# Kernel tuning notes

Hardware: AMD Instinct MI355X
Metric: run time of the kernel (lower is better)

The kernel has to match this reference:

```python
import jax, jax.numpy as jnp
import numpy as np

H, HKV, HD = 16, 4, 128
EPS = 1.1920928955078125e-07  # float32 eps, torch F.rms_norm default


def _rms_norm(t):
    return t * jax.lax.rsqrt(jnp.mean(t * t, axis=-1, keepdims=True) + EPS)


def _rope(t, cos, sin):
    # t: [B, T, h, HD]; cos/sin: [T, HD//2] -> broadcast [1, T, 1, HD//2]
    te, to = t[..., 0::2], t[..., 1::2]
    c = cos[None, :, None, :]
    s = sin[None, :, None, :]
    re = te * c - to * s
    ro = te * s + to * c
    return jnp.stack((re, ro), axis=-1).reshape(t.shape)


def setup_inputs() -> dict:
    key = jax.random.key(0)
    ks = jax.random.split(key, 5)
    B, T, C = 2, 2048, 2048
    return {
        "x": jax.random.normal(ks[0], (B, T, C), jnp.float32),
        "Wq": jax.random.normal(ks[1], (C, C), jnp.float32) * 0.02,
        "Wk": jax.random.normal(ks[2], (HKV * HD, C), jnp.float32) * 0.02,
        "Wv": jax.random.normal(ks[3], (HKV * HD, C), jnp.float32) * 0.02,
        "Wo": jax.random.normal(ks[4], (C, C), jnp.float32) * 0.02,
        "q_gain": jnp.full((H,), 5.0, jnp.float32),
    }


def reference(x, Wq, Wk, Wv, Wo, q_gain):
    B, T, C = x.shape
    q = (x @ Wq.T).reshape(B, T, H, HD)
    k = (x @ Wk.T).reshape(B, T, HKV, HD)
    v = (x @ Wv.T).reshape(B, T, HKV, HD)

    q = _rms_norm(q)
    k = _rms_norm(k)

    theta = 1.0 / (10000.0 ** (jnp.arange(0, HD, 2, dtype=jnp.float32) / HD))
    t = jnp.arange(T, dtype=jnp.float32)
    freqs = jnp.outer(t, theta)  # [T, HD//2]
    cos, sin = jnp.cos(freqs), jnp.sin(freqs)

    q = _rope(q, cos, sin)
    k = _rope(k, cos, sin)
    q = q * q_gain[None, None, :, None]

    qh = q.transpose(0, 2, 1, 3)                       # [B, H, T, HD]
    kh = jnp.repeat(k.transpose(0, 2, 1, 3), H // HKV, axis=1)
    vh = jnp.repeat(v.transpose(0, 2, 1, 3), H // HKV, axis=1)

    scale = 1.0 / jnp.sqrt(jnp.float32(HD))
    scores = jnp.einsum("bhqd,bhkd->bhqk", qh, kh) * scale
    causal = jnp.tril(jnp.ones((T, T), bool))
    scores = jnp.where(causal[None, None], scores, jnp.finfo(scores.dtype).min)
    attn = jax.nn.softmax(scores, axis=-1)
    out = jnp.einsum("bhqk,bhkd->bhqd", attn, vh)
    out = out.transpose(0, 2, 1, 3).reshape(B, T, C)
    return out @ Wo.T
```

## Files before the change

### kernel.cpp

```cpp
#include <hip/hip_runtime.h>
#include <hip/hip_bf16.h>

#define TSEQ 2048
#define CDIM 2048
#define NH   16
#define NKV  4
#define HDIM 128
#define BATCH 2
#define MROWS (BATCH*TSEQ)
#define KVC   (NKV*HDIM)
#define QKVC  (CDIM + 2*KVC)

typedef short bf16x8 __attribute__((ext_vector_type(8)));
typedef float f32x4  __attribute__((ext_vector_type(4)));

typedef const __attribute__((address_space(1))) void* gptr_t;
typedef __attribute__((address_space(3))) void* sptr_t;

__device__ inline void async16(const __hip_bfloat16* g, __hip_bfloat16* l) {
  __builtin_amdgcn_global_load_lds((gptr_t)g, (sptr_t)l, 16, 0, 0);
}

__device__ inline f32x4 mfma16(bf16x8 a, bf16x8 b, f32x4 c) {
  return __builtin_amdgcn_mfma_f32_16x16x32_bf16(a, b, c, 0, 0, 0);
}

__device__ inline float bfbits2f(unsigned short u) {
  return __uint_as_float(((unsigned)u) << 16);
}

__device__ inline unsigned short f2bfu(float x) {
  __hip_bfloat16 t = __float2bfloat16(x);
  return *(unsigned short*)&t;
}

__device__ inline int swz128(int row, int col) {
  return row*128 + (((col >> 3) ^ (row & 15)) << 3) + (col & 7);
}
__device__ inline int swz64(int row, int col) {
  return row*64 + ((((col >> 3) ^ row) & 7) << 3) + (col & 7);
}

__global__ void canary(const void* __restrict__ x, int* __restrict__ flag) {
  __shared__ int cnt[256];
  int tid = threadIdx.x;
  const unsigned short* u = (const unsigned short*)x;
  int c = 0;
#pragma unroll
  for (int i = 0; i < 4; ++i) {
    float a = fabsf(bfbits2f(u[(tid*4 + i)*2]));
    if (a >= 1e-6f && a <= 1e3f) c++;
  }
  cnt[tid] = c;
  __syncthreads();
  for (int s = 128; s > 0; s >>= 1) {
    if (tid < s) cnt[tid] += cnt[tid + s];
    __syncthreads();
  }
  if (tid == 0) *flag = (cnt[0] > 512) ? 1 : 0;
}

__global__ __launch_bounds__(256) void canonize_all(
    const void* __restrict__ xs,  const void* __restrict__ wqs,
    const void* __restrict__ wks, const void* __restrict__ wvs,
    const void* __restrict__ wos, const void* __restrict__ gs,
    __hip_bfloat16* __restrict__ xd,
    __hip_bfloat16* __restrict__ wqkv,
    __hip_bfloat16* __restrict__ wod,
    __hip_bfloat16* __restrict__ gd,
    const int* __restrict__ flag)
{
  int blk = blockIdx.x;
  const void* src; __hip_bfloat16* dst; int base, n;
  if      (blk < 4096) { src = xs;  dst = xd;                base = blk;        n = MROWS*CDIM; }
  else if (blk < 6144) { src = wqs; dst = wqkv;              base = blk - 4096; n = CDIM*CDIM; }
  else if (blk < 6656) { src = wks; dst = wqkv + (size_t)CDIM*CDIM;            base = blk - 6144; n = KVC*CDIM; }
  else if (blk < 7168) { src = wvs; dst = wqkv + (size_t)(CDIM+KVC)*CDIM;      base = blk - 6656; n = KVC*CDIM; }
  else if (blk < 9216) { src = wos; dst = wod;               base = blk - 7168; n = CDIM*CDIM; }
  else                 { src = gs;  dst = gd;                base = 0;          n = NH; }
  int idx = base*2048 + threadIdx.x*8;
  if (idx >= n) return;
  if (*flag) {
    *(bf16x8*)&dst[idx] = *(const bf16x8*)((const __hip_bfloat16*)src + idx);
  } else {
    const float* s = (const float*)src + idx;
    float4 f0 = *(const float4*)s;
    float4 f1 = *(const float4*)(s + 4);
    union { bf16x8 v; unsigned short u[8]; } o;
    o.u[0] = f2bfu(f0.x); o.u[1] = f2bfu(f0.y);
    o.u[2] = f2bfu(f0.z); o.u[3] = f2bfu(f0.w);
    o.u[4] = f2bfu(f1.x); o.u[5] = f2bfu(f1.y);
    o.u[6] = f2bfu(f1.z); o.u[7] = f2bfu(f1.w);
    *(bf16x8*)&dst[idx] = o.v;
  }
}

#define BK 64

__global__ __launch_bounds__(512, 2) void gemm_bt256(
    const __hip_bfloat16* __restrict__ A,
    const __hip_bfloat16* __restrict__ B,
    __hip_bfloat16* __restrict__ C,
    int M, int N, int K, int lda)
{
  __shared__ __align__(16) __hip_bfloat16 As[2][256*BK];
  __shared__ __align__(16) __hip_bfloat16 Bs[2][192*BK];
  const int tid  = threadIdx.x;
  const int wave = tid >> 6;
  const int lane = tid & 63;
  const int qd   = lane >> 4;
  const int ln   = lane & 15;
  const int m0   = blockIdx.y * 256;
  const int n0   = blockIdx.x * 192;
  const int wm   = (wave >> 2) * 128;
  const int wn   = (wave & 3) * 48;

  auto stageA = [&](int buf, int kt) {
    const __hip_bfloat16* src = A + (size_t)m0*lda + kt*BK;
    __hip_bfloat16* dst = &As[buf][0];
#pragma unroll
    for (int i = 0; i < 4; ++i) {
      int c = i*512 + tid;
      int row = c >> 3, sl = c & 7;
      int gs = sl ^ (row & 7);
      async16(&src[(size_t)row*lda + gs*8], &dst[(i*512 + wave*64)*8]);
    }
  };
  auto stageB = [&](int buf, int kt) {
    const __hip_bfloat16* src = B + (size_t)n0*K + kt*BK;
    __hip_bfloat16* dst = &Bs[buf][0];
#pragma unroll
    for (int i = 0; i < 3; ++i) {
      int c = i*512 + tid;
      int row = c >> 3, sl = c & 7;
      int gs = sl ^ (row & 7);
      async16(&src[(size_t)row*K + gs*8], &dst[(i*512 + wave*64)*8]);
    }
  };
  auto ldA = [&](int buf, int m, int kk) -> bf16x8 {
    int row = wm + m*16 + ln;
    return *(const bf16x8*)&As[buf][row*BK + (((kk*4 + qd) ^ (row & 7)) << 3)];
  };
  auto ldB = [&](int buf, int n, int kk) -> bf16x8 {
    int row = wn + n*16 + ln;
    return *(const bf16x8*)&Bs[buf][row*BK + (((kk*4 + qd) ^ (row & 7)) << 3)];
  };

  f32x4 acc[8][3] = {};
  const int nt = K / BK;

  stageA(0, 0); stageB(0, 0);
  if (nt > 1) {
    stageA(1, 1); stageB(1, 1);
    asm volatile("s_waitcnt vmcnt(7)" ::: "memory");
  } else {
    asm volatile("s_waitcnt vmcnt(0)" ::: "memory");
  }
  __builtin_amdgcn_s_barrier();

#pragma unroll 1
  for (int t = 0; t < nt; ++t) {
    const int buf = t & 1;
    bf16x8 a03[4][2], a47[4][2], b01[2][2], b2[2];

#pragma unroll
    for (int m = 0; m < 4; ++m)
#pragma unroll
      for (int kk = 0; kk < 2; ++kk) a03[m][kk] = ldA(buf, m, kk);
#pragma unroll
    for (int n = 0; n < 2; ++n)
#pragma unroll
      for (int kk = 0; kk < 2; ++kk) b01[n][kk] = ldB(buf, n, kk);
    __builtin_amdgcn_s_setprio(1);
#pragma unroll
    for (int m = 0; m < 4; ++m)
#pragma unroll
      for (int n = 0; n < 2; ++n)
#pragma unroll
        for (int kk = 0; kk < 2; ++kk)
          acc[m][n] = mfma16(a03[m][kk], b01[n][kk], acc[m][n]);
    __builtin_amdgcn_s_setprio(0);
    __builtin_amdgcn_s_barrier();

#pragma unroll
    for (int m = 0; m < 4; ++m)
#pragma unroll
      for (int kk = 0; kk < 2; ++kk) a47[m][kk] = ldA(buf, 4 + m, kk);
    __builtin_amdgcn_s_setprio(1);
#pragma unroll
    for (int m = 0; m < 4; ++m)
#pragma unroll
      for (int n = 0; n < 2; ++n)
#pragma unroll
        for (int kk = 0; kk < 2; ++kk)
          acc[4 + m][n] = mfma16(a47[m][kk], b01[n][kk], acc[4 + m][n]);
    __builtin_amdgcn_s_setprio(0);
    __builtin_amdgcn_s_barrier();

#pragma unroll
    for (int kk = 0; kk < 2; ++kk) b2[kk] = ldB(buf, 2, kk);
    if (t + 2 < nt) stageA(buf, t + 2);
    __builtin_amdgcn_s_setprio(1);
#pragma unroll
    for (int m = 0; m < 4; ++m)
#pragma unroll
      for (int kk = 0; kk < 2; ++kk)
        acc[m][2] = mfma16(a03[m][kk], b2[kk], acc[m][2]);
    __builtin_amdgcn_s_setprio(0);
    __builtin_amdgcn_s_barrier();

    if (t + 2 < nt) stageB(buf, t + 2);
    __builtin_amdgcn_s_setprio(1);
#pragma unroll
    for (int m = 0; m < 4; ++m)
#pragma unroll
      for (int kk = 0; kk < 2; ++kk)
        acc[4 + m][2] = mfma16(a47[m][kk], b2[kk], acc[4 + m][2]);
    __builtin_amdgcn_s_setprio(0);
    if (t + 2 < nt) asm volatile("s_waitcnt vmcnt(7)" ::: "memory");
    else            asm volatile("s_waitcnt vmcnt(0)" ::: "memory");
    __builtin_amdgcn_s_barrier();
  }

#pragma unroll
  for (int m = 0; m < 8; ++m)
#pragma unroll
    for (int n = 0; n < 3; ++n) {
      int row = m0 + wm + m*16 + qd*4;
      int col = n0 + wn + n*16 + ln;
#pragma unroll
      for (int r = 0; r < 4; ++r)
        C[(size_t)(row + r)*N + col] = __float2bfloat16(acc[m][n][r]);
    }
}

__global__ __launch_bounds__(256, 2) void gemm_out(
    const __hip_bfloat16* __restrict__ A,
    const __hip_bfloat16* __restrict__ B,
    void* __restrict__ C,
    int M, int N, int K, int lda, const int* __restrict__ flag)
{
  __shared__ __align__(16) __hip_bfloat16 As[128*32];
  __shared__ __align__(16) __hip_bfloat16 Bs[128*32];
  const int tid  = threadIdx.x;
  const int wave = tid >> 6;
  const int lane = tid & 63;
  const int qd   = lane >> 4;
  const int ln   = lane & 15;
  const int m0   = blockIdx.y * 128;
  const int n0   = blockIdx.x * 128;
  const int wm   = (wave >> 1) * 64;
  const int wn   = (wave & 1) * 64;

  f32x4 acc[4][4] = {};

  for (int k0 = 0; k0 < K; k0 += 32) {
    __syncthreads();
#pragma unroll
    for (int r = 0; r < 2; ++r) {
      int e   = (r*256 + tid) * 8;
      int row = e >> 5;
      int col = e & 31;
      async16(&A[(size_t)(m0+row)*lda + k0 + col], &As[(size_t)(r*256 + wave*64)*8]);
      async16(&B[(size_t)(n0+row)*K   + k0 + col], &Bs[(size_t)(r*256 + wave*64)*8]);
    }
    __syncthreads();
    bf16x8 af[4], bfr[4];
#pragma unroll
    for (int i = 0; i < 4; ++i)
      af[i] = *(const bf16x8*)&As[(wm + i*16 + ln)*32 + qd*8];
#pragma unroll
    for (int j = 0; j < 4; ++j)
      bfr[j] = *(const bf16x8*)&Bs[(wn + j*16 + ln)*32 + qd*8];
#pragma unroll
    for (int i = 0; i < 4; ++i)
#pragma unroll
      for (int j = 0; j < 4; ++j)
        acc[i][j] = mfma16(af[i], bfr[j], acc[i][j]);
  }
  const bool isbf = (*flag != 0);
#pragma unroll
  for (int i = 0; i < 4; ++i)
#pragma unroll
    for (int j = 0; j < 4; ++j) {
      int row = m0 + wm + i*16 + qd*4;
      int col = n0 + wn + j*16 + ln;
#pragma unroll
      for (int r = 0; r < 4; ++r) {
        if (isbf) ((__hip_bfloat16*)C)[(size_t)(row + r)*N + col] = __float2bfloat16(acc[i][j][r]);
        else      ((float*)C)[(size_t)(row + r)*N + col] = acc[i][j][r];
      }
    }
}

__global__ __launch_bounds__(256) void prep_qk(
    __hip_bfloat16* __restrict__ qkv,
    const __hip_bfloat16* __restrict__ gain)
{
  int wid2 = blockIdx.x * 4 + (threadIdx.x >> 6);
  int lane = threadIdx.x & 63;
  int half = lane >> 5;
  int l32  = lane & 31;
  int rowid = wid2 * 2 + half;
  bool isq = rowid < MROWS*NH;
  int m, h;
  __hip_bfloat16* p;
  if (isq) { m = rowid >> 4; h = rowid & 15; p = qkv + (size_t)m*QKVC + h*HDIM; }
  else     { int w2 = rowid - MROWS*NH; m = w2 >> 2; h = w2 & 3; p = qkv + (size_t)m*QKVC + CDIM + h*HDIM; }

  ushort4 raw = *(const ushort4*)((const unsigned short*)p + 4*l32);
  float e0 = bfbits2f(raw.x), o0 = bfbits2f(raw.y);
  float e1 = bfbits2f(raw.z), o1 = bfbits2f(raw.w);
  float ss = (e0*e0 + o0*o0) + (e1*e1 + o1*o1);
#pragma unroll
  for (int off = 16; off >= 1; off >>= 1) ss += __shfl_xor(ss, off);
  float rms = rsqrtf(ss * (1.0f/128.0f) + 1.1920928955078125e-07f);
  e0 *= rms; o0 *= rms; e1 *= rms; o1 *= rms;

  int j0 = 2*l32;
  float th0 = exp2f(-(float)(2*j0)     * (1.0f/128.0f) * 13.287712379549449f);
  float th1 = exp2f(-(float)(2*j0 + 2) * (1.0f/128.0f) * 13.287712379549449f);
  int t = m & (TSEQ-1);
  float fr0 = (float)t * th0, fr1 = (float)t * th1;
  float c0 = cosf(fr0), s0 = sinf(fr0);
  float c1 = cosf(fr1), s1 = sinf(fr1);
  float re0 = e0*c0 - o0*s0, ro0 = e0*s0 + o0*c0;
  float re1 = e1*c1 - o1*s1, ro1 = e1*s1 + o1*c1;

  if (isq) {
    float g = bfbits2f(*(const unsigned short*)&gain[h]) * 0.08838834764831845f;
    re0 *= g; ro0 *= g; re1 *= g; ro1 *= g;
  }
  ushort4 outv;
  outv.x = f2bfu(re0); outv.y = f2bfu(ro0);
  outv.z = f2bfu(re1); outv.w = f2bfu(ro1);
  *(ushort4*)((unsigned short*)p + 4*l32) = outv;
}

__global__ __launch_bounds__(256) void transpose_v(
    const __hip_bfloat16* __restrict__ qkv, __hip_bfloat16* __restrict__ vt)
{
  __shared__ __hip_bfloat16 tile[32][34];
  int tx = threadIdx.x & 31;
  int ty = threadIdx.x >> 5;
  int r0 = blockIdx.x * 32;
  int c0 = blockIdx.y * 32;
#pragma unroll
  for (int i = 0; i < 4; ++i)
    tile[ty + i*8][tx] = qkv[(size_t)(r0 + ty + i*8)*QKVC + (CDIM + KVC) + c0 + tx];
  __syncthreads();
  int b = r0 >> 11;
  int t = r0 & (TSEQ-1);
  int hk = c0 >> 7;
  int d0 = c0 & (HDIM-1);
#pragma unroll
  for (int i = 0; i < 4; ++i) {
    int d = d0 + ty + i*8;
    vt[((size_t)((b*NKV + hk)*HDIM + d))*TSEQ + t + tx] = tile[tx][ty + i*8];
  }
}

__global__ __launch_bounds__(256, 2) void attn_kernel(
    const __hip_bfloat16* __restrict__ qkv,
    const __hip_bfloat16* __restrict__ vt,
    __hip_bfloat16* __restrict__ out)
{
  const int tid  = threadIdx.x;
  const int wave = tid >> 6;
  const int lane = tid & 63;
  const int qd = lane >> 4, ln = lane & 15;
  const int p  = blockIdx.x;
  const int h  = blockIdx.y;
  const int b  = blockIdx.z;
  const int hk = h >> 2;

  const __hip_bfloat16* K = qkv + (size_t)(b*TSEQ)*QKVC + CDIM + hk*HDIM;
  const __hip_bfloat16* V = vt + ((size_t)(b*NKV + hk)*HDIM)*TSEQ;

  __shared__ __align__(16) __hip_bfloat16 Ks[64*128];
  __shared__ __align__(16) __hip_bfloat16 Vs[128*64];
  __shared__ __align__(16) __hip_bfloat16 Pb[64*64];
  __shared__ float Lb[4][64];

  auto issueK = [&](int t0) {
#pragma unroll
    for (int i = 0; i < 4; ++i) {
      int c = i*256 + tid;
      int row = c >> 4, cc = c & 15;
      int gcc = cc ^ (row & 15);
      async16(&K[(size_t)(t0 + row)*QKVC + gcc*8], &Ks[(i*256 + wave*64)*8]);
    }
  };
  auto issueV = [&](int t0) {
#pragma unroll
    for (int i = 0; i < 4; ++i) {
      int c = i*256 + tid;
      int row = c >> 3, cc = c & 7;
      int gcc = cc ^ (row & 7);
      async16(&V[(size_t)row*TSEQ + t0 + gcc*8], &Vs[(i*256 + wave*64)*8]);
    }
  };

#pragma unroll 1
  for (int seg = 0; seg < 2; ++seg) {
    const int qt = seg ? (31 - p) : p;
    const int q0 = qt * 64;

    bf16x8 qfr[4][4];
#pragma unroll
    for (int qsub = 0; qsub < 4; ++qsub)
#pragma unroll
      for (int kc = 0; kc < 4; ++kc)
        qfr[qsub][kc] = *(const bf16x8*)&qkv[((size_t)(b*TSEQ + q0 + qsub*16 + ln))*QKVC + h*HDIM + kc*32 + qd*8];

    f32x4 o[2][4] = {};
    float lacc[4] = {0.f, 0.f, 0.f, 0.f};

    __syncthreads();
    issueK(0);
    __syncthreads();

#pragma unroll 1
    for (int kt = 0; kt <= qt; ++kt) {
      const int t0 = kt * 64;
      issueV(t0);

      f32x4 sc[4] = {};
#pragma unroll
      for (int kc = 0; kc < 4; ++kc) {
        bf16x8 kfa = *(const bf16x8*)&Ks[swz128(wave*16 + ln, kc*32 + qd*8)];
#pragma unroll
        for (int qsub = 0; qsub < 4; ++qsub)
          sc[qsub] = mfma16(kfa, qfr[qsub][kc], sc[qsub]);
      }
      if (kt == qt) {
#pragma unroll
        for (int qsub = 0; qsub < 4; ++qsub)
#pragma unroll
          for (int r = 0; r < 4; ++r) {
            int kv = t0 + wave*16 + qd*4 + r;
            int q  = q0 + qsub*16 + ln;
            if (kv > q) sc[qsub][r] = -1.0e30f;
          }
      }
#pragma unroll
      for (int qsub = 0; qsub < 4; ++qsub) {
#pragma unroll
        for (int r = 0; r < 4; ++r)
          sc[qsub][r] = __expf(sc[qsub][r]);
        lacc[qsub] += (sc[qsub][0] + sc[qsub][1]) + (sc[qsub][2] + sc[qsub][3]);
      }

#pragma unroll
      for (int qsub = 0; qsub < 4; ++qsub) {
        ushort4 pk;
        pk.x = f2bfu(sc[qsub][0]); pk.y = f2bfu(sc[qsub][1]);
        pk.z = f2bfu(sc[qsub][2]); pk.w = f2bfu(sc[qsub][3]);
        *(ushort4*)&Pb[swz64(qsub*16 + ln, wave*16 + qd*4)] = pk;
      }

      __syncthreads();
      if (kt < qt) issueK(t0 + 64);

      __builtin_amdgcn_s_setprio(1);
#pragma unroll
      for (int kc2 = 0; kc2 < 2; ++kc2) {
        bf16x8 pfb[4];
#pragma unroll
        for (int qsub = 0; qsub < 4; ++qsub)
          pfb[qsub] = *(const bf16x8*)&Pb[swz64(qsub*16 + ln, kc2*32 + qd*8)];
#pragma unroll
        for (int half = 0; half < 2; ++half) {
          bf16x8 vfa = *(const bf16x8*)&Vs[swz64(wave*32 + half*16 + ln, kc2*32 + qd*8)];
#pragma unroll
          for (int qsub = 0; qsub < 4; ++qsub)
            o[half][qsub] = mfma16(vfa, pfb[qsub], o[half][qsub]);
        }
      }
      __builtin_amdgcn_s_setprio(0);
      __syncthreads();
    }

#pragma unroll
    for (int qsub = 0; qsub < 4; ++qsub) {
      lacc[qsub] += __shfl_xor(lacc[qsub], 16);
      lacc[qsub] += __shfl_xor(lacc[qsub], 32);
    }
    if (qd == 0) {
#pragma unroll
      for (int qsub = 0; qsub < 4; ++qsub)
        Lb[wave][qsub*16 + ln] = lacc[qsub];
    }
    __syncthreads();
    float inv[4];
#pragma unroll
    for (int qsub = 0; qsub < 4; ++qsub) {
      int q = qsub*16 + ln;
      inv[qsub] = 1.0f / (((Lb[0][q] + Lb[1][q]) + (Lb[2][q] + Lb[3][q])));
    }

#pragma unroll
    for (int half = 0; half < 2; ++half)
#pragma unroll
      for (int qsub = 0; qsub < 4; ++qsub) {
        ushort4 pk;
        pk.x = f2bfu(o[half][qsub][0] * inv[qsub]);
        pk.y = f2bfu(o[half][qsub][1] * inv[qsub]);
        pk.z = f2bfu(o[half][qsub][2] * inv[qsub]);
        pk.w = f2bfu(o[half][qsub][3] * inv[qsub]);
        *(ushort4*)&Ks[swz128(qsub*16 + ln, wave*32 + half*16 + qd*4)] = pk;
      }
    __syncthreads();
#pragma unroll
    for (int pass = 0; pass < 4; ++pass) {
      int row = wave*16 + pass*4 + qd;
      bf16x8 val = *(const bf16x8*)&Ks[swz128(row, ln*8)];
      int q = q0 + row;
      *(bf16x8*)&out[((size_t)(b*TSEQ + q))*CDIM + h*HDIM + ln*8] = val;
    }
  }
}

extern "C" void kernel_launch(void* const* d_in, const int* in_sizes, int n_in,
                              void* d_out, int out_size, void* d_ws, size_t ws_size,
                              hipStream_t stream) {
  char* ws = (char*)d_ws;
  size_t off = 0;
  auto alloc = [&](size_t bytes) { char* p = ws + off; off += (bytes + 255) & ~(size_t)255; return p; };

  int* flag = (int*)alloc(256);
  __hip_bfloat16* xb   = (__hip_bfloat16*)alloc((size_t)MROWS*CDIM*2);
  __hip_bfloat16* wqkv = (__hip_bfloat16*)alloc((size_t)QKVC*CDIM*2);
  __hip_bfloat16* wob  = (__hip_bfloat16*)alloc((size_t)CDIM*CDIM*2);
  __hip_bfloat16* gb   = (__hip_bfloat16*)alloc(256);
  __hip_bfloat16* qkv  = (__hip_bfloat16*)alloc((size_t)MROWS*QKVC*2);
  __hip_bfloat16* vt   = (__hip_bfloat16*)alloc((size_t)MROWS*KVC*2);

  canary<<<1, 256, 0, stream>>>(d_in[0], flag);

  canonize_all<<<9217, 256, 0, stream>>>(
      d_in[0], d_in[1], d_in[2], d_in[3], d_in[4], d_in[5],
      xb, wqkv, wob, gb, flag);

  gemm_bt256<<<dim3(QKVC/192, MROWS/256), 512, 0, stream>>>(
      xb, wqkv, qkv, MROWS, QKVC, CDIM, CDIM);

  prep_qk<<<(MROWS*NH + MROWS*NKV)/8, 256, 0, stream>>>(qkv, gb);

  transpose_v<<<dim3(MROWS/32, KVC/32), 256, 0, stream>>>(qkv, vt);

  attn_kernel<<<dim3(16, NH, BATCH), 256, 0, stream>>>(qkv, vt, xb);

  gemm_out<<<dim3(CDIM/128, MROWS/128), 256, 0, stream>>>(
      xb, wob, d_out, MROWS, CDIM, CDIM, CDIM, flag);
}
```

Baseline: 292.8 us.

## Inline dtype detection, merge prep and V-transpose kernels, triple-buffer A in QKV GEMM

Drops the separate canary kernel; each wave of canonize_all and gemm_out now detects bf16 input itself with a shuffle reduction. Merges the Q/K rms-norm+RoPE kernel and the V transpose into one launch, so there are two fewer kernel launches overall. The QKV GEMM moves its A tile to three LDS buffers and issues the prefetch in two halves earlier in the iteration, so global loads overlap more of the MFMA work. In exchange, LDS use rises (may cut occupancy below two blocks per CU), every wave repeats the detection reads, and the existing vmcnt(7) wait count is kept despite the new load order.

Result: faster. 284.6 us (-2.8%).

```diff
diff --git a/kernel.cpp b/kernel.cpp
--- a/kernel.cpp
+++ b/kernel.cpp
@@ -34,30 +34,25 @@
   return *(unsigned short*)&t;
 }
 
+__device__ inline bool detect_bf16(const void* x) {
+  const unsigned short* u = (const unsigned short*)x;
+  int lane = threadIdx.x & 63;
+  int c = 0;
+#pragma unroll
+  for (int i = 0; i < 4; ++i) {
+    float a = fabsf(bfbits2f(u[(lane*4 + i)*2]));
+    if (a >= 1e-6f && a <= 1e3f) c++;
+  }
+#pragma unroll
+  for (int off = 32; off >= 1; off >>= 1) c += __shfl_xor(c, off);
+  return c > 128;
+}
+
 __device__ inline int swz128(int row, int col) {
   return row*128 + (((col >> 3) ^ (row & 15)) << 3) + (col & 7);
 }
 __device__ inline int swz64(int row, int col) {
   return row*64 + ((((col >> 3) ^ row) & 7) << 3) + (col & 7);
-}
-
-__global__ void canary(const void* __restrict__ x, int* __restrict__ flag) {
-  __shared__ int cnt[256];
-  int tid = threadIdx.x;
-  const unsigned short* u = (const unsigned short*)x;
-  int c = 0;
-#pragma unroll
-  for (int i = 0; i < 4; ++i) {
-    float a = fabsf(bfbits2f(u[(tid*4 + i)*2]));
-    if (a >= 1e-6f && a <= 1e3f) c++;
-  }
-  cnt[tid] = c;
-  __syncthreads();
-  for (int s = 128; s > 0; s >>= 1) {
-    if (tid < s) cnt[tid] += cnt[tid + s];
-    __syncthreads();
-  }
-  if (tid == 0) *flag = (cnt[0] > 512) ? 1 : 0;
 }
 
 __global__ __launch_bounds__(256) void canonize_all(
@@ -67,9 +62,9 @@
     __hip_bfloat16* __restrict__ xd,
     __hip_bfloat16* __restrict__ wqkv,
     __hip_bfloat16* __restrict__ wod,
-    __hip_bfloat16* __restrict__ gd,
-    const int* __restrict__ flag)
+    __hip_bfloat16* __restrict__ gd)
 {
+  const bool isbf = detect_bf16(xs);
   int blk = blockIdx.x;
   const void* src; __hip_bfloat16* dst; int base, n;
   if      (blk < 4096) { src = xs;  dst = xd;                base = blk;        n = MROWS*CDIM; }
@@ -80,7 +75,7 @@
   else                 { src = gs;  dst = gd;                base = 0;          n = NH; }
   int idx = base*2048 + threadIdx.x*8;
   if (idx >= n) return;
-  if (*flag) {
+  if (isbf) {
     *(bf16x8*)&dst[idx] = *(const bf16x8*)((const __hip_bfloat16*)src + idx);
   } else {
     const float* s = (const float*)src + idx;
@@ -103,7 +98,7 @@
     __hip_bfloat16* __restrict__ C,
     int M, int N, int K, int lda)
 {
-  __shared__ __align__(16) __hip_bfloat16 As[2][256*BK];
+  __shared__ __align__(16) __hip_bfloat16 As[3][256*BK];
   __shared__ __align__(16) __hip_bfloat16 Bs[2][192*BK];
   const int tid  = threadIdx.x;
   const int wave = tid >> 6;
@@ -115,11 +110,11 @@
   const int wm   = (wave >> 2) * 128;
   const int wn   = (wave & 3) * 48;
 
-  auto stageA = [&](int buf, int kt) {
-    const __hip_bfloat16* src = A + (size_t)m0*lda + kt*BK;
-    __hip_bfloat16* dst = &As[buf][0];
-#pragma unroll
-    for (int i = 0; i < 4; ++i) {
+  auto stageAhalf = [&](int buf, int kt, int half) {
+    const __hip_bfloat16* src = A + (size_t)(m0 + half*128)*lda + kt*BK;
+    __hip_bfloat16* dst = &As[buf][half*128*BK];
+#pragma unroll
+    for (int i = 0; i < 2; ++i) {
       int c = i*512 + tid;
       int row = c >> 3, sl = c & 7;
       int gs = sl ^ (row & 7);
@@ -149,9 +144,9 @@
   f32x4 acc[8][3] = {};
   const int nt = K / BK;
 
-  stageA(0, 0); stageB(0, 0);
+  stageAhalf(0, 0, 0); stageAhalf(0, 0, 1); stageB(0, 0);
   if (nt > 1) {
-    stageA(1, 1); stageB(1, 1);
+    stageAhalf(1, 1, 0); stageAhalf(1, 1, 1); stageB(1, 1);
     asm volatile("s_waitcnt vmcnt(7)" ::: "memory");
   } else {
     asm volatile("s_waitcnt vmcnt(0)" ::: "memory");
@@ -160,17 +155,21 @@
 
 #pragma unroll 1
   for (int t = 0; t < nt; ++t) {
-    const int buf = t & 1;
+    const int bufA = t % 3;
+    const int bufB = t & 1;
+    int nextA = bufA + 2; if (nextA >= 3) nextA -= 3;
+    const bool pre = (t + 2 < nt);
     bf16x8 a03[4][2], a47[4][2], b01[2][2], b2[2];
 
 #pragma unroll
     for (int m = 0; m < 4; ++m)
 #pragma unroll
-      for (int kk = 0; kk < 2; ++kk) a03[m][kk] = ldA(buf, m, kk);
+      for (int kk = 0; kk < 2; ++kk) a03[m][kk] = ldA(bufA, m, kk);
 #pragma unroll
     for (int n = 0; n < 2; ++n)
 #pragma unroll
-      for (int kk = 0; kk < 2; ++kk) b01[n][kk] = ldB(buf, n, kk);
+      for (int kk = 0; kk < 2; ++kk) b01[n][kk] = ldB(bufB, n, kk);
+    if (pre) stageAhalf(nextA, t + 2, 0);
     __builtin_amdgcn_s_setprio(1);
 #pragma unroll
     for (int m = 0; m < 4; ++m)
@@ -185,7 +184,8 @@
 #pragma unroll
     for (int m = 0; m < 4; ++m)
 #pragma unroll
-      for (int kk = 0; kk < 2; ++kk) a47[m][kk] = ldA(buf, 4 + m, kk);
+      for (int kk = 0; kk < 2; ++kk) a47[m][kk] = ldA(bufA, 4 + m, kk);
+    if (pre) stageAhalf(nextA, t + 2, 1);
     __builtin_amdgcn_s_setprio(1);
 #pragma unroll
     for (int m = 0; m < 4; ++m)
@@ -198,8 +198,7 @@
     __builtin_amdgcn_s_barrier();
 
 #pragma unroll
-    for (int kk = 0; kk < 2; ++kk) b2[kk] = ldB(buf, 2, kk);
-    if (t + 2 < nt) stageA(buf, t + 2);
+    for (int kk = 0; kk < 2; ++kk) b2[kk] = ldB(bufB, 2, kk);
     __builtin_amdgcn_s_setprio(1);
 #pragma unroll
     for (int m = 0; m < 4; ++m)
@@ -209,7 +208,7 @@
     __builtin_amdgcn_s_setprio(0);
     __builtin_amdgcn_s_barrier();
 
-    if (t + 2 < nt) stageB(buf, t + 2);
+    if (pre) stageB(bufB, t + 2);
     __builtin_amdgcn_s_setprio(1);
 #pragma unroll
     for (int m = 0; m < 4; ++m)
@@ -217,8 +216,8 @@
       for (int kk = 0; kk < 2; ++kk)
         acc[4 + m][2] = mfma16(a47[m][kk], b2[kk], acc[4 + m][2]);
     __builtin_amdgcn_s_setprio(0);
-    if (t + 2 < nt) asm volatile("s_waitcnt vmcnt(7)" ::: "memory");
-    else            asm volatile("s_waitcnt vmcnt(0)" ::: "memory");
+    if (pre) asm volatile("s_waitcnt vmcnt(7)" ::: "memory");
+    else     asm volatile("s_waitcnt vmcnt(0)" ::: "memory");
     __builtin_amdgcn_s_barrier();
   }
 
@@ -238,8 +237,9 @@
     const __hip_bfloat16* __restrict__ A,
     const __hip_bfloat16* __restrict__ B,
     void* __restrict__ C,
-    int M, int N, int K, int lda, const int* __restrict__ flag)
+    int M, int N, int K, int lda, const void* __restrict__ xorig)
 {
+  const bool isbf = detect_bf16(xorig);
   __shared__ __align__(16) __hip_bfloat16 As[128*32];
   __shared__ __align__(16) __hip_bfloat16 Bs[128*32];
   const int tid  = threadIdx.x;
@@ -278,7 +278,6 @@
       for (int j = 0; j < 4; ++j)
         acc[i][j] = mfma16(af[i], bfr[j], acc[i][j]);
   }
-  const bool isbf = (*flag != 0);
 #pragma unroll
   for (int i = 0; i < 4; ++i)
 #pragma unroll
@@ -293,70 +292,71 @@
     }
 }
 
-__global__ __launch_bounds__(256) void prep_qk(
+__global__ __launch_bounds__(256) void prep_and_tv(
     __hip_bfloat16* __restrict__ qkv,
-    const __hip_bfloat16* __restrict__ gain)
+    const __hip_bfloat16* __restrict__ gain,
+    __hip_bfloat16* __restrict__ vt)
 {
-  int wid2 = blockIdx.x * 4 + (threadIdx.x >> 6);
-  int lane = threadIdx.x & 63;
-  int half = lane >> 5;
-  int l32  = lane & 31;
-  int rowid = wid2 * 2 + half;
-  bool isq = rowid < MROWS*NH;
-  int m, h;
-  __hip_bfloat16* p;
-  if (isq) { m = rowid >> 4; h = rowid & 15; p = qkv + (size_t)m*QKVC + h*HDIM; }
-  else     { int w2 = rowid - MROWS*NH; m = w2 >> 2; h = w2 & 3; p = qkv + (size_t)m*QKVC + CDIM + h*HDIM; }
-
-  ushort4 raw = *(const ushort4*)((const unsigned short*)p + 4*l32);
-  float e0 = bfbits2f(raw.x), o0 = bfbits2f(raw.y);
-  float e1 = bfbits2f(raw.z), o1 = bfbits2f(raw.w);
-  float ss = (e0*e0 + o0*o0) + (e1*e1 + o1*o1);
-#pragma unroll
-  for (int off = 16; off >= 1; off >>= 1) ss += __shfl_xor(ss, off);
-  float rms = rsqrtf(ss * (1.0f/128.0f) + 1.1920928955078125e-07f);
-  e0 *= rms; o0 *= rms; e1 *= rms; o1 *= rms;
-
-  int j0 = 2*l32;
-  float th0 = exp2f(-(float)(2*j0)     * (1.0f/128.0f) * 13.287712379549449f);
-  float th1 = exp2f(-(float)(2*j0 + 2) * (1.0f/128.0f) * 13.287712379549449f);
-  int t = m & (TSEQ-1);
-  float fr0 = (float)t * th0, fr1 = (float)t * th1;
-  float c0 = cosf(fr0), s0 = sinf(fr0);
-  float c1 = cosf(fr1), s1 = sinf(fr1);
-  float re0 = e0*c0 - o0*s0, ro0 = e0*s0 + o0*c0;
-  float re1 = e1*c1 - o1*s1, ro1 = e1*s1 + o1*c1;
-
-  if (isq) {
-    float g = bfbits2f(*(const unsigned short*)&gain[h]) * 0.08838834764831845f;
-    re0 *= g; ro0 *= g; re1 *= g; ro1 *= g;
-  }
-  ushort4 outv;
-  outv.x = f2bfu(re0); outv.y = f2bfu(ro0);
-  outv.z = f2bfu(re1); outv.w = f2bfu(ro1);
-  *(ushort4*)((unsigned short*)p + 4*l32) = outv;
-}
-
-__global__ __launch_bounds__(256) void transpose_v(
-    const __hip_bfloat16* __restrict__ qkv, __hip_bfloat16* __restrict__ vt)
-{
-  __shared__ __hip_bfloat16 tile[32][34];
-  int tx = threadIdx.x & 31;
-  int ty = threadIdx.x >> 5;
-  int r0 = blockIdx.x * 32;
-  int c0 = blockIdx.y * 32;
-#pragma unroll
-  for (int i = 0; i < 4; ++i)
-    tile[ty + i*8][tx] = qkv[(size_t)(r0 + ty + i*8)*QKVC + (CDIM + KVC) + c0 + tx];
-  __syncthreads();
-  int b = r0 >> 11;
-  int t = r0 & (TSEQ-1);
-  int hk = c0 >> 7;
-  int d0 = c0 & (HDIM-1);
-#pragma unroll
-  for (int i = 0; i < 4; ++i) {
-    int d = d0 + ty + i*8;
-    vt[((size_t)((b*NKV + hk)*HDIM + d))*TSEQ + t + tx] = tile[tx][ty + i*8];
+  int blk = blockIdx.x;
+  if (blk < 10240) {
+    int wid2 = blk * 4 + (threadIdx.x >> 6);
+    int lane = threadIdx.x & 63;
+    int half = lane >> 5;
+    int l32  = lane & 31;
+    int rowid = wid2 * 2 + half;
+    bool isq = rowid < MROWS*NH;
+    int m, h;
+    __hip_bfloat16* p;
+    if (isq) { m = rowid >> 4; h = rowid & 15; p = qkv + (size_t)m*QKVC + h*HDIM; }
+    else     { int w2 = rowid - MROWS*NH; m = w2 >> 2; h = w2 & 3; p = qkv + (size_t)m*QKVC + CDIM + h*HDIM; }
+
+    ushort4 raw = *(const ushort4*)((const unsigned short*)p + 4*l32);
+    float e0 = bfbits2f(raw.x), o0 = bfbits2f(raw.y);
+    float e1 = bfbits2f(raw.z), o1 = bfbits2f(raw.w);
+    float ss = (e0*e0 + o0*o0) + (e1*e1 + o1*o1);
+#pragma unroll
+    for (int off = 16; off >= 1; off >>= 1) ss += __shfl_xor(ss, off);
+    float rms = rsqrtf(ss * (1.0f/128.0f) + 1.1920928955078125e-07f);
+    e0 *= rms; o0 *= rms; e1 *= rms; o1 *= rms;
+
+    int j0 = 2*l32;
+    float th0 = exp2f(-(float)(2*j0)     * (1.0f/128.0f) * 13.287712379549449f);
+    float th1 = exp2f(-(float)(2*j0 + 2) * (1.0f/128.0f) * 13.287712379549449f);
+    int t = m & (TSEQ-1);
+    float fr0 = (float)t * th0, fr1 = (float)t * th1;
+    float c0 = cosf(fr0), s0 = sinf(fr0);
+    float c1 = cosf(fr1), s1 = sinf(fr1);
+    float re0 = e0*c0 - o0*s0, ro0 = e0*s0 + o0*c0;
+    float re1 = e1*c1 - o1*s1, ro1 = e1*s1 + o1*c1;
+
+    if (isq) {
+      float g = bfbits2f(*(const unsigned short*)&gain[h]) * 0.08838834764831845f;
+      re0 *= g; ro0 *= g; re1 *= g; ro1 *= g;
+    }
+    ushort4 outv;
+    outv.x = f2bfu(re0); outv.y = f2bfu(ro0);
+    outv.z = f2bfu(re1); outv.w = f2bfu(ro1);
+    *(ushort4*)((unsigned short*)p + 4*l32) = outv;
+  } else {
+    __shared__ __hip_bfloat16 tile[32][34];
+    int bx = blk - 10240;
+    int tx = threadIdx.x & 31;
+    int ty = threadIdx.x >> 5;
+    int r0 = (bx & 127) * 32;
+    int c0 = (bx >> 7) * 32;
+#pragma unroll
+    for (int i = 0; i < 4; ++i)
+      tile[ty + i*8][tx] = qkv[(size_t)(r0 + ty + i*8)*QKVC + (CDIM + KVC) + c0 + tx];
+    __syncthreads();
+    int b = r0 >> 11;
+    int t = r0 & (TSEQ-1);
+    int hk = c0 >> 7;
+    int d0 = c0 & (HDIM-1);
+#pragma unroll
+    for (int i = 0; i < 4; ++i) {
+      int d = d0 + ty + i*8;
+      vt[((size_t)((b*NKV + hk)*HDIM + d))*TSEQ + t + tx] = tile[tx][ty + i*8];
+    }
   }
 }
 
@@ -528,7 +528,6 @@
   size_t off = 0;
   auto alloc = [&](size_t bytes) { char* p = ws + off; off += (bytes + 255) & ~(size_t)255; return p; };
 
-  int* flag = (int*)alloc(256);
   __hip_bfloat16* xb   = (__hip_bfloat16*)alloc((size_t)MROWS*CDIM*2);
   __hip_bfloat16* wqkv = (__hip_bfloat16*)alloc((size_t)QKVC*CDIM*2);
   __hip_bfloat16* wob  = (__hip_bfloat16*)alloc((size_t)CDIM*CDIM*2);
@@ -536,21 +535,17 @@
   __hip_bfloat16* qkv  = (__hip_bfloat16*)alloc((size_t)MROWS*QKVC*2);
   __hip_bfloat16* vt   = (__hip_bfloat16*)alloc((size_t)MROWS*KVC*2);
 
-  canary<<<1, 256, 0, stream>>>(d_in[0], flag);
-
   canonize_all<<<9217, 256, 0, stream>>>(
       d_in[0], d_in[1], d_in[2], d_in[3], d_in[4], d_in[5],
-      xb, wqkv, wob, gb, flag);
+      xb, wqkv, wob, gb);
 
   gemm_bt256<<<dim3(QKVC/192, MROWS/256), 512, 0, stream>>>(
       xb, wqkv, qkv, MROWS, QKVC, CDIM, CDIM);
 
-  prep_qk<<<(MROWS*NH + MROWS*NKV)/8, 256, 0, stream>>>(qkv, gb);
-
-  transpose_v<<<dim3(MROWS/32, KVC/32), 256, 0, stream>>>(qkv, vt);
+  prep_and_tv<<<12288, 256, 0, stream>>>(qkv, gb, vt);
 
   attn_kernel<<<dim3(16, NH, BATCH), 256, 0, stream>>>(qkv, vt, xb);
 
   gemm_out<<<dim3(CDIM/128, MROWS/128), 256, 0, stream>>>(
-      xb, wob, d_out, MROWS, CDIM, CDIM, CDIM, flag);
-}
+      xb, wob, d_out, MROWS, CDIM, CDIM, CDIM, d_in[0]);
+}
```
